# Performance work log

Hardware: AMD Instinct MI355X
Metric: run time of the kernel (lower is better)

The kernel has to match this reference:

```python
import jax, jax.numpy as jnp
import numpy as np


def _gcn_conv(x, W, b, src, dst, n):
    # x: [N, F_in] -> project first (dense GEMM), then normalized scatter-add.
    h = x @ W  # [N, F_out]
    deg = jax.ops.segment_sum(jnp.ones_like(dst, dtype=h.dtype), dst, num_segments=n)  # in-degree incl. self loops
    inv_sqrt = jax.lax.rsqrt(deg)  # deg >= 1 because self loops were added
    norm = inv_sqrt[src] * inv_sqrt[dst]  # [E+N]
    out = jax.ops.segment_sum(h[src] * norm[:, None], dst, num_segments=n)  # [N, F_out]
    return out + b


def setup_inputs() -> dict:
    key = jax.random.key(0)
    k1, k2, k3, k4 = jax.random.split(key, 4)
    N, E, F_IN, H, C = 10000, 160000, 3703, 1024, 6
    x = jax.random.normal(k1, (N, F_IN), dtype=jnp.float32)
    edge_index = jax.random.randint(k2, (2, E), 0, N, dtype=jnp.int64)
    # Glorot-style init for weights
    W1 = jax.random.normal(k3, (F_IN, H), dtype=jnp.float32) * np.float32(1.0 / np.sqrt(F_IN))
    W2 = jax.random.normal(k4, (H, C), dtype=jnp.float32) * np.float32(1.0 / np.sqrt(H))
    b1 = jnp.zeros((H,), dtype=jnp.float32)
    b2 = jnp.zeros((C,), dtype=jnp.float32)
    return {"x": x, "edge_index": edge_index, "W1": W1, "b1": b1, "W2": W2, "b2": b2}


def reference(x, edge_index, W1, b1, W2, b2):
    n = x.shape[0]
    # GCNConv adds self loops; degree normalization D^{-1/2}(A+I)D^{-1/2}
    loop = jnp.arange(n, dtype=edge_index.dtype)
    src = jnp.concatenate([edge_index[0], loop])
    dst = jnp.concatenate([edge_index[1], loop])
    h = _gcn_conv(x, W1, b1, src, dst, n)
    h = jax.nn.relu(h)
    # dropout is identity in eval mode
    h = _gcn_conv(h, W2, b2, src, dst, n)
    return jax.nn.log_softmax(h, axis=1)
```

## Files before the change

kernel.cpp:

```cpp
#include <hip/hip_runtime.h>
#include <stdint.h>

typedef unsigned short u16;
typedef unsigned int u32;
typedef __bf16 bf16x8 __attribute__((ext_vector_type(8)));
typedef float f32x4 __attribute__((ext_vector_type(4)));

#define N_NODES 10000
#define N_EDGES 160000
#define F_IN    3703
#define HDIM    1024
#define CDIM    6
#define KP      3712
#define KT      58

static __device__ __forceinline__ u16 f2bf(float f) {
    u32 u = __builtin_bit_cast(u32, f);
    u32 r = (u + 0x7fffu + ((u >> 16) & 1u)) >> 16;
    return (u16)r;
}
static __device__ __forceinline__ float bf2f(u16 b) {
    return __builtin_bit_cast(float, ((u32)b) << 16);
}

#define GL2LDS(g, l) __builtin_amdgcn_global_load_lds(                         \
    (const __attribute__((address_space(1))) void*)(g),                        \
    (__attribute__((address_space(3))) void*)(l), 16, 0, 0)

__global__ void k_count(const int* __restrict__ ei, int* counts) {
    int e = blockIdx.x * 256 + threadIdx.x;
    if (e < N_EDGES) {
        int dst = ei[N_EDGES + e];
        atomicAdd(&counts[dst], 1);
    }
}

__global__ void k_scan(const int* __restrict__ counts, int* __restrict__ offsets,
                       float* __restrict__ inv_sqrt) {
    __shared__ int wsum[16];
    int t = threadIdx.x, lane = t & 63, wv = t >> 6;
    int local[10];
    int s = 0;
    #pragma unroll
    for (int i = 0; i < 10; i++) {
        int idx = t * 10 + i;
        int v = (idx < N_NODES) ? counts[idx] : 0;
        local[i] = s; s += v;
    }
    int incl = s;
    #pragma unroll
    for (int off = 1; off < 64; off <<= 1) {
        int v = __shfl_up(incl, off);
        if (lane >= off) incl += v;
    }
    if (lane == 63) wsum[wv] = incl;
    __syncthreads();
    if (t == 0) {
        int a = 0;
        #pragma unroll
        for (int i = 0; i < 16; i++) { int v = wsum[i]; wsum[i] = a; a += v; }
    }
    __syncthreads();
    int base = wsum[wv] + incl - s;
    #pragma unroll
    for (int i = 0; i < 10; i++) {
        int idx = t * 10 + i;
        if (idx < N_NODES) {
            offsets[idx] = base + local[i];
            inv_sqrt[idx] = rsqrtf((float)(counts[idx] + 1));
        }
    }
    if (t == 1023) offsets[N_NODES] = wsum[15] + incl;
}

__global__ void k_fill(const int* __restrict__ ei, const int* __restrict__ offsets,
                       int* cursor, int* __restrict__ edge_src) {
    int e = blockIdx.x * 256 + threadIdx.x;
    if (e < N_EDGES) {
        int src = ei[e];
        int dst = ei[N_EDGES + e];
        int pos = atomicAdd(&cursor[dst], 1);
        edge_src[offsets[dst] + pos] = src;
    }
}

__global__ void k_cvt_w1t(const float* __restrict__ W1, u16* __restrict__ BT) {
    __shared__ u16 tile[64][66];
    int k0 = blockIdx.x * 64, n0 = blockIdx.y * 64;
    int tx = threadIdx.x & 63, ty = threadIdx.x >> 6;
    #pragma unroll
    for (int i = 0; i < 16; i++) {
        int kk = ty + i * 4;
        int k = k0 + kk;
        float v = (k < F_IN) ? W1[(size_t)k * HDIM + n0 + tx] : 0.f;
        tile[kk][tx] = f2bf(v);
    }
    __syncthreads();
    #pragma unroll
    for (int i = 0; i < 16; i++) {
        int nn = ty + i * 4;
        BT[(size_t)(n0 + nn) * KP + k0 + tx] = tile[tx][nn];
    }
}

__global__ __launch_bounds__(256) void k_gemm1(const float* __restrict__ x,
                                               const u16* __restrict__ BT,
                                               u16* __restrict__ H1) {
    __shared__ __align__(16) float Asf[128 * 64];
    __shared__ __align__(16) u16 Bs[128 * 64];
    const int tid = threadIdx.x;
    const int lane = tid & 63;
    const int wid = tid >> 6;
    const int wm = wid >> 1, wn = wid & 1;

    const u32 orig = (u32)blockIdx.y * 8u + (u32)blockIdx.x;
    const u32 lin  = (orig & 7u) * 79u + (orig >> 3);
    const int bm = (int)(lin >> 3);
    const int bn = (int)(lin & 7u);

    u32 aflat[8]; int adst[8];
    #pragma unroll
    for (int j = 0; j < 8; j++) {
        int q = wid * 8 + j;
        int e = q * 256 + lane * 4;
        int row = e >> 6, c = e & 63;
        int csrc = c ^ ((row & 7) << 3);
        aflat[j] = (u32)(bm * 128 + row) * F_IN + csrc;
        adst[j] = q * 256;
    }
    const u32 XMAX = (u32)N_NODES * F_IN - 4;

    int srowB[4], scolB[4], sdstB[4];
    #pragma unroll
    for (int j = 0; j < 4; j++) {
        int q = wid * 4 + j;
        int e = q * 512 + lane * 8;
        int row = e >> 6, c = e & 63;
        srowB[j] = row;
        scolB[j] = c ^ ((row & 7) << 3);
        sdstB[j] = q * 512;
    }
    const u16* Bbase = BT + (size_t)bn * 128 * KP;

    f32x4 acc[4][4];
    #pragma unroll
    for (int i = 0; i < 4; i++)
        #pragma unroll
        for (int j = 0; j < 4; j++)
            acc[i][j] = (f32x4)0.f;

    for (int kt = 0; kt < KT; ++kt) {
        const int k0 = kt * 64;
        #pragma unroll
        for (int j = 0; j < 8; j++) {
            u32 flat = aflat[j] + (u32)k0;
            flat = flat > XMAX ? XMAX : flat;
            GL2LDS(x + flat, Asf + adst[j]);
        }
        #pragma unroll
        for (int j = 0; j < 4; j++)
            GL2LDS(Bbase + (size_t)srowB[j] * KP + k0 + scolB[j], Bs + sdstB[j]);
        __syncthreads();

        const int rA = wm * 64 + (lane & 15);
        const int rB = wn * 64 + (lane & 15);
        const int cb = (lane >> 4) << 3;
        #pragma unroll
        for (int kk = 0; kk < 2; kk++) {
            bf16x8 av[4], bv[4];
            const int cc = kk * 32 + cb;
            #pragma unroll
            for (int i = 0; i < 4; i++) {
                int r = rA + i * 16;
                int pos = r * 64 + (cc ^ ((r & 7) << 3));
                f32x4 lo = *(const f32x4*)(Asf + pos);
                f32x4 hi = *(const f32x4*)(Asf + pos + 4);
                bf16x8 a;
                #pragma unroll
                for (int m = 0; m < 4; m++) {
                    a[m]     = (__bf16)lo[m];
                    a[m + 4] = (__bf16)hi[m];
                }
                av[i] = a;
                int r2 = rB + i * 16;
                bv[i] = *(const bf16x8*)(Bs + r2 * 64 + (cc ^ ((r2 & 7) << 3)));
            }
            #pragma unroll
            for (int i = 0; i < 4; i++)
                #pragma unroll
                for (int j = 0; j < 4; j++)
                    acc[i][j] = __builtin_amdgcn_mfma_f32_16x16x32_bf16(
                        av[i], bv[j], acc[i][j], 0, 0, 0);
        }
        __syncthreads();
    }

    const int cr = (lane >> 4) * 4;
    const int ccol = lane & 15;
    #pragma unroll
    for (int i = 0; i < 4; i++) {
        #pragma unroll
        for (int j = 0; j < 4; j++) {
            #pragma unroll
            for (int r = 0; r < 4; r++) {
                int row = bm * 128 + wm * 64 + i * 16 + cr + r;
                if (row < N_NODES) {
                    int col = bn * 128 + wn * 64 + j * 16 + ccol;
                    H1[(size_t)row * HDIM + col] = f2bf(acc[i][j][r]);
                }
            }
        }
    }
}

__global__ void k_agg1g2(const u16* __restrict__ H1, const int* __restrict__ offsets,
                         const int* __restrict__ edge_src, const float* __restrict__ inv_sqrt,
                         const float* __restrict__ b1, const float* __restrict__ W2,
                         float* __restrict__ H2) {
    __shared__ float red[4][8];
    int node = blockIdx.x;
    int t = threadIdx.x;
    int lane = t & 63, wv = t >> 6;
    int f = t * 4;
    float is_n = inv_sqrt[node];
    float a0, a1, a2, a3;
    {
        float w = is_n * is_n;
        ushort4 v = *(const ushort4*)(H1 + (size_t)node * HDIM + f);
        a0 = bf2f(v.x) * w; a1 = bf2f(v.y) * w; a2 = bf2f(v.z) * w; a3 = bf2f(v.w) * w;
    }
    int beg = offsets[node], end = offsets[node + 1];
    for (int base = beg; base < end; base += 64) {
        int idx = base + lane;
        int sv = (idx < end) ? edge_src[idx] : 0;
        float pv = (idx < end) ? inv_sqrt[sv] : 0.f;
        int cnt = min(64, end - base);
        for (int i = 0; i < cnt; i++) {
            int s = __shfl(sv, i);
            float w = __shfl(pv, i) * is_n;
            ushort4 v = *(const ushort4*)(H1 + (size_t)s * HDIM + f);
            a0 += bf2f(v.x) * w; a1 += bf2f(v.y) * w;
            a2 += bf2f(v.z) * w; a3 += bf2f(v.w) * w;
        }
    }
    float4 bb = *(const float4*)(b1 + f);
    float z0 = fmaxf(a0 + bb.x, 0.f);
    float z1 = fmaxf(a1 + bb.y, 0.f);
    float z2 = fmaxf(a2 + bb.z, 0.f);
    float z3 = fmaxf(a3 + bb.w, 0.f);
    float acc[6];
    #pragma unroll
    for (int c = 0; c < 6; c++)
        acc[c] = z0 * W2[(size_t)f * 6 + c] + z1 * W2[(size_t)(f + 1) * 6 + c]
               + z2 * W2[(size_t)(f + 2) * 6 + c] + z3 * W2[(size_t)(f + 3) * 6 + c];
    #pragma unroll
    for (int c = 0; c < 6; c++) {
        #pragma unroll
        for (int off = 32; off > 0; off >>= 1) acc[c] += __shfl_xor(acc[c], off);
    }
    if (lane == 0) {
        #pragma unroll
        for (int c = 0; c < 6; c++) red[wv][c] = acc[c];
    }
    __syncthreads();
    if (t < 6) {
        float s = red[0][t] + red[1][t] + red[2][t] + red[3][t];
        H2[(size_t)node * CDIM + t] = s;
    }
}

__global__ void k_agg2(const float* __restrict__ H2, const int* __restrict__ offsets,
                       const int* __restrict__ edge_src, const float* __restrict__ inv_sqrt,
                       const float* __restrict__ b2, float* __restrict__ out) {
    int gt = blockIdx.x * 256 + threadIdx.x;
    int node = gt >> 3, sub = gt & 7;
    if (node >= N_NODES) return;
    float is_n = inv_sqrt[node];
    float acc[6] = {0.f, 0.f, 0.f, 0.f, 0.f, 0.f};
    int beg = offsets[node], end = offsets[node + 1];
    for (int e = beg + sub; e < end; e += 8) {
        int s = edge_src[e];
        float w = inv_sqrt[s] * is_n;
        #pragma unroll
        for (int c = 0; c < 6; c++) acc[c] += H2[(size_t)s * CDIM + c] * w;
    }
    if (sub == 0) {
        float w = is_n * is_n;
        #pragma unroll
        for (int c = 0; c < 6; c++) acc[c] += H2[(size_t)node * CDIM + c] * w;
    }
    #pragma unroll
    for (int off = 1; off < 8; off <<= 1) {
        #pragma unroll
        for (int c = 0; c < 6; c++) acc[c] += __shfl_xor(acc[c], off);
    }
    if (sub == 0) {
        float z[6];
        #pragma unroll
        for (int c = 0; c < 6; c++) z[c] = acc[c] + b2[c];
        float m = z[0];
        #pragma unroll
        for (int c = 1; c < 6; c++) m = fmaxf(m, z[c]);
        float ssum = 0.f;
        #pragma unroll
        for (int c = 0; c < 6; c++) ssum += __expf(z[c] - m);
        float l = m + logf(ssum);
        #pragma unroll
        for (int c = 0; c < 6; c++) out[(size_t)node * CDIM + c] = z[c] - l;
    }
}

extern "C" void kernel_launch(void* const* d_in, const int* in_sizes, int n_in,
                              void* d_out, int out_size, void* d_ws, size_t ws_size,
                              hipStream_t stream) {
    const float* x  = (const float*)d_in[0];
    const int*   ei = (const int*)d_in[1];
    const float* W1 = (const float*)d_in[2];
    const float* b1 = (const float*)d_in[3];
    const float* W2 = (const float*)d_in[4];
    const float* b2 = (const float*)d_in[5];
    float* out = (float*)d_out;

    char* ws = (char*)d_ws;
    size_t off = 0;
    auto alloc = [&](size_t bytes) -> void* {
        void* p = ws + off;
        off += (bytes + 255) & ~(size_t)255;
        return p;
    };
    u16* BT       = (u16*)alloc((size_t)HDIM * KP * 2);
    u16* H1       = (u16*)alloc((size_t)N_NODES * HDIM * 2);
    int* counts   = (int*)alloc(N_NODES * 4);
    int* cursor   = (int*)alloc(N_NODES * 4);
    int* offsets  = (int*)alloc((N_NODES + 1) * 4);
    float* inv_sq = (float*)alloc(N_NODES * 4);
    int* edge_src = (int*)alloc(N_EDGES * 4);
    float* H2 = (float*)BT;

    hipMemsetAsync(counts, 0, N_NODES * 4, stream);
    hipMemsetAsync(cursor, 0, N_NODES * 4, stream);
    k_count<<<(N_EDGES + 255) / 256, 256, 0, stream>>>(ei, counts);
    k_scan<<<1, 1024, 0, stream>>>(counts, offsets, inv_sq);
    k_fill<<<(N_EDGES + 255) / 256, 256, 0, stream>>>(ei, offsets, cursor, edge_src);

    dim3 gT(KP / 64, HDIM / 64);
    k_cvt_w1t<<<gT, 256, 0, stream>>>(W1, BT);

    dim3 gG(HDIM / 128, 79);
    k_gemm1<<<gG, 256, 0, stream>>>(x, BT, H1);

    k_agg1g2<<<N_NODES, 256, 0, stream>>>(H1, offsets, edge_src, inv_sq, b1, W2, H2);
    k_agg2<<<(N_NODES * 8 + 255) / 256, 256, 0, stream>>>(H2, offsets, edge_src, inv_sq, b2, out);
}
```

Baseline: 249.5 us.

## Register-prefetch A tile, convert to bf16 once, store bf16 in LDS

The fp32 A tile is now loaded from global memory into registers one k-step ahead. It is converted to bf16 once and written to a bf16 LDS buffer, replacing the direct global-to-LDS fp32 copy and the per-wave conversion at MFMA time. This halves LDS footprint and LDS read traffic for A and overlaps the next global load with compute. The costs are more VGPRs, unaligned vector global loads, and the loss of the async LDS-direct load path for A.

New measurement: 313.8 us. 25.7% more time.

```diff
diff --git a/kernel.cpp b/kernel.cpp
--- a/kernel.cpp
+++ b/kernel.cpp
@@ -5,6 +5,7 @@
 typedef unsigned int u32;
 typedef __bf16 bf16x8 __attribute__((ext_vector_type(8)));
 typedef float f32x4 __attribute__((ext_vector_type(4)));
+typedef float f32x4u __attribute__((ext_vector_type(4), aligned(4)));
 
 #define N_NODES 10000
 #define N_EDGES 160000
@@ -106,7 +107,7 @@
 __global__ __launch_bounds__(256) void k_gemm1(const float* __restrict__ x,
                                                const u16* __restrict__ BT,
                                                u16* __restrict__ H1) {
-    __shared__ __align__(16) float Asf[128 * 64];
+    __shared__ __align__(16) u16 As[128 * 64];
     __shared__ __align__(16) u16 Bs[128 * 64];
     const int tid = threadIdx.x;
     const int lane = tid & 63;
@@ -118,17 +119,34 @@
     const int bm = (int)(lin >> 3);
     const int bn = (int)(lin & 7u);
 
-    u32 aflat[8]; int adst[8];
-    #pragma unroll
-    for (int j = 0; j < 8; j++) {
-        int q = wid * 8 + j;
-        int e = q * 256 + lane * 4;
-        int row = e >> 6, c = e & 63;
-        int csrc = c ^ ((row & 7) << 3);
-        aflat[j] = (u32)(bm * 128 + row) * F_IN + csrc;
-        adst[j] = q * 256;
-    }
+    const int ar0 = tid >> 4;
+    const int ac0 = (tid & 15) * 4;
+    u32 arow_flat[8];
+    #pragma unroll
+    for (int p = 0; p < 8; p++)
+        arow_flat[p] = (u32)(bm * 128 + ar0 + p * 16) * F_IN + ac0;
     const u32 XMAX = (u32)N_NODES * F_IN - 4;
+    f32x4u va[8];
+    auto loadA = [&](int kt) {
+        const u32 kb = (u32)(kt * 64);
+        #pragma unroll
+        for (int p = 0; p < 8; p++) {
+            u32 flat = arow_flat[p] + kb;
+            flat = flat > XMAX ? XMAX : flat;
+            va[p] = *(const f32x4u*)(x + flat);
+        }
+    };
+    auto writeA = [&]() {
+        #pragma unroll
+        for (int p = 0; p < 8; p++) {
+            int r = ar0 + p * 16;
+            int c = ac0 ^ ((r & 7) << 3);
+            ushort4 o;
+            o.x = f2bf(va[p].x); o.y = f2bf(va[p].y);
+            o.z = f2bf(va[p].z); o.w = f2bf(va[p].w);
+            *(ushort4*)&As[r * 64 + c] = o;
+        }
+    };
 
     int srowB[4], scolB[4], sdstB[4];
     #pragma unroll
@@ -149,18 +167,17 @@
         for (int j = 0; j < 4; j++)
             acc[i][j] = (f32x4)0.f;
 
+    loadA(0);
+
     for (int kt = 0; kt < KT; ++kt) {
         const int k0 = kt * 64;
         #pragma unroll
-        for (int j = 0; j < 8; j++) {
-            u32 flat = aflat[j] + (u32)k0;
-            flat = flat > XMAX ? XMAX : flat;
-            GL2LDS(x + flat, Asf + adst[j]);
-        }
-        #pragma unroll
         for (int j = 0; j < 4; j++)
             GL2LDS(Bbase + (size_t)srowB[j] * KP + k0 + scolB[j], Bs + sdstB[j]);
+        writeA();
         __syncthreads();
+
+        if (kt + 1 < KT) loadA(kt + 1);
 
         const int rA = wm * 64 + (lane & 15);
         const int rB = wn * 64 + (lane & 15);
@@ -172,16 +189,7 @@
             #pragma unroll
             for (int i = 0; i < 4; i++) {
                 int r = rA + i * 16;
-                int pos = r * 64 + (cc ^ ((r & 7) << 3));
-                f32x4 lo = *(const f32x4*)(Asf + pos);
-                f32x4 hi = *(const f32x4*)(Asf + pos + 4);
-                bf16x8 a;
-                #pragma unroll
-                for (int m = 0; m < 4; m++) {
-                    a[m]     = (__bf16)lo[m];
-                    a[m + 4] = (__bf16)hi[m];
-                }
-                av[i] = a;
+                av[i] = *(const bf16x8*)(As + r * 64 + (cc ^ ((r & 7) << 3)));
                 int r2 = rB + i * 16;
                 bv[i] = *(const bf16x8*)(Bs + r2 * 64 + (cc ^ ((r2 & 7) << 3)));
             }
```
